# Kernel tuning notes

Hardware: AMD Instinct MI355X
Metric: run time of the kernel (lower is better)

The kernel has to match this reference:

```python
import jax, jax.numpy as jnp
import numpy as np

B, H, W, N, DIM = 2, 64, 64, 4, 128
HEADS = 4
SPLIT = 2          # split_size; idx == 0 -> window = (H, SPLIT)
HEAD_DIM = DIM // HEADS
SCALE = HEAD_DIM ** -0.5


def setup_inputs() -> dict:
    key = jax.random.key(0)
    k1, k2, k3, k4 = jax.random.split(key, 4)
    query = jax.random.normal(k1, (B, H, W, N, DIM), jnp.float32)
    key_t = jax.random.normal(k2, (B, H, W, N, DIM), jnp.float32)
    value = jax.random.normal(k3, (B, H, W, N, DIM), jnp.float32)
    conv_w = jax.random.normal(k4, (DIM, 1, 3, 3), jnp.float32) * 0.1  # depthwise get_v
    return {"query": query, "key": key_t, "value": value, "conv_w": conv_w}


def _im2cswin(x, hs, ws, heads):
    # b (i hs) (j ws) n (h d) -> (b i j) h (hs ws n) d
    b, ht, wd, n, c = x.shape
    i, j = ht // hs, wd // ws
    d = c // heads
    x = x.reshape(b, i, hs, j, ws, n, heads, d)
    x = x.transpose(0, 1, 3, 6, 2, 4, 5, 7)  # b i j h hs ws n d
    return x.reshape(b * i * j, heads, hs * ws * n, d)


def _cswin_forward(query, key, value, conv_w):
    b, ht, wd, n, c = query.shape
    hs, ws = ht, SPLIT  # idx == 0; ht % hs == 0 and wd % ws == 0 -> no padding
    i, j = ht // hs, wd // ws
    Bw = b * i * j

    q = _im2cswin(query, hs, ws, HEADS) * SCALE
    k = _im2cswin(key, hs, ws, HEADS)

    # --- get_rpe (locally-enhanced positional encoding on value) ---
    # value windows: b i j n c hs ws
    vw = value.reshape(b, i, hs, j, ws, n, c).transpose(0, 1, 3, 5, 6, 2, 4)
    vw = vw.reshape(Bw, n, c, hs, ws)
    vimg = vw.reshape(Bw * n, c, hs, ws)
    conv = jax.lax.conv_general_dilated(
        vimg, conv_w, window_strides=(1, 1), padding=((1, 1), (1, 1)),
        dimension_numbers=("NCHW", "OIHW", "NCHW"), feature_group_count=c)
    conv = conv.reshape(Bw, n, c, hs, ws)
    rpe = conv.sum(axis=1, keepdims=True)  # Bw 1 c hs ws
    # subtract center-tap contribution of all other candidates at same pixel
    mask_n = (1.0 - jnp.eye(n, dtype=query.dtype)) * -1.0  # (n, n)
    center = conv_w[:, 0, 1, 1]  # (c,)
    tmp = vw * center[None, None, :, None, None]
    tmp = jnp.einsum("jk,bkdhw->bjdhw", mask_n, tmp)
    rpe = rpe + tmp  # Bw n c hs ws

    def to_tokens(t):
        # b n (h d) hs ws -> b h (hs ws n) d
        t = t.reshape(Bw, n, HEADS, HEAD_DIM, hs, ws)
        t = t.transpose(0, 2, 4, 5, 1, 3)
        return t.reshape(Bw, HEADS, hs * ws * n, HEAD_DIM)

    rpe = to_tokens(rpe)
    v = to_tokens(vw)

    # --- window attention mask: block self-edges between candidates at same pixel ---
    L = hs * ws * n
    tok = jnp.arange(L)
    sp = tok // n  # spatial index of each token
    amask = jnp.where(sp[:, None] == sp[None, :], -jnp.inf, 0.0)
    amask = jnp.where(tok[:, None] == tok[None, :], 0.0, amask).astype(query.dtype)

    attn = jnp.einsum("bhic,bhjc->bhij", q, k) + amask[None, None]
    attn = jax.nn.softmax(attn, axis=-1)
    x = jnp.einsum("bhij,bhjc->bhic", attn, v) + rpe

    # (b i j) h (hs ws n) d -> b (i hs) (j ws) n (h d)
    x = x.reshape(b, i, j, HEADS, hs, ws, n, HEAD_DIM)
    x = x.transpose(0, 1, 4, 2, 5, 6, 3, 7).reshape(b, ht, wd, n, c)
    return x


def reference(query, key, value, conv_w):
    return _cswin_forward(query, key, value, conv_w)
```

## Files before the change

### kernel.cpp

```cpp
#include <hip/hip_runtime.h>
#include <stdint.h>


typedef __bf16 bf16x8 __attribute__((ext_vector_type(8)));
typedef float f32x4 __attribute__((ext_vector_type(4)));
typedef float f32x2 __attribute__((ext_vector_type(2)));

#if __has_builtin(__builtin_amdgcn_exp2f)
#define EXP2F __builtin_amdgcn_exp2f
#else
#define EXP2F exp2f
#endif

union U4 { uint4 u; bf16x8 v; unsigned short s[8]; };

__device__ __forceinline__ float bf2f(unsigned short h){ union{unsigned u;float f;}x; x.u=((unsigned)h)<<16; return x.f; }

__device__ __forceinline__ unsigned cvtpk(float lo, float hi){
  unsigned d;
  asm("v_cvt_pk_bf16_f32 %0, %1, %2" : "=v"(d) : "v"(lo), "v"(hi));
  return d;
}
__device__ __forceinline__ U4 pack8(float4 a, float4 b){
  U4 r;
  r.u.x = cvtpk(a.x, a.y); r.u.y = cvtpk(a.z, a.w);
  r.u.z = cvtpk(b.x, b.y); r.u.w = cvtpk(b.z, b.w);
  return r;
}

__device__ __forceinline__ void pls32(unsigned &a, unsigned &b){
#if __has_builtin(__builtin_amdgcn_permlane32_swap)
  auto r = __builtin_amdgcn_permlane32_swap(a, b, false, false);
  a = r[0]; b = r[1];
#else
  unsigned sa_ = __shfl_xor(a, 32), sb_ = __shfl_xor(b, 32);
  bool hi = ((threadIdx.x & 32) != 0);
  unsigned na = hi ? sb_ : a, nb = hi ? b : sa_;
  a = na; b = nb;
#endif
}
__device__ __forceinline__ void pls16(unsigned &a, unsigned &b){
#if __has_builtin(__builtin_amdgcn_permlane16_swap)
  auto r = __builtin_amdgcn_permlane16_swap(a, b, false, false);
  a = r[0]; b = r[1];
#else
  unsigned sa_ = __shfl_xor(a, 16), sb_ = __shfl_xor(b, 16);
  bool hi = ((threadIdx.x & 16) != 0);
  unsigned na = hi ? sb_ : a, nb = hi ? b : sa_;
  a = na; b = nb;
#endif
}

__device__ __forceinline__ void xpose_p(const unsigned w[4][2], U4& ap0, U4& ap1)
{
  unsigned a0 = w[0][0], b0 = w[1][0]; pls32(a0, b0); pls16(a0, b0);
  unsigned a1 = w[0][1], b1 = w[1][1]; pls32(a1, b1); pls16(a1, b1);
  ap0.u.x = a0; ap0.u.y = a1; ap0.u.z = b0; ap0.u.w = b1;
  unsigned c0 = w[2][0], d0 = w[3][0]; pls32(c0, d0); pls16(c0, d0);
  unsigned c1 = w[2][1], d1 = w[3][1]; pls32(c1, d1); pls16(c1, d1);
  ap1.u.x = c0; ap1.u.y = c1; ap1.u.z = d0; ap1.u.w = d1;
}

#define C_SCALE 0.25506953149031837f
#define M_SHIFT 20.0f

#define VT_OFF 0
#define KS_OFF 32768
#define LDS_BYTES 65536

__global__ __launch_bounds__(1024, 1) void cswin_attn_kernel(
    const float* __restrict__ qg,
    const float* __restrict__ kg,
    const float* __restrict__ vg,
    const float* __restrict__ cwg,
    float* __restrict__ outg)
{
  __shared__ __align__(16) unsigned char smem[LDS_BYTES];
  const int tid = threadIdx.x;
  const int lane = tid & 63;
  const int wave = tid >> 6;
  const int qd = lane >> 4;
  const int n  = lane & 15;

  const int swn = (n & 7) << 2;
  const int xb0 = ((4 * qd) ^ swn) << 2;
  const int xb1 = xb0 ^ 64;

  const int bh = blockIdx.x;
  const int head = bh & 3;
  const int bw = bh >> 2;
  const int b  = bw >> 5;
  const int jj = bw & 31;

  const size_t wbase = (size_t)b * 2097152 + (size_t)(jj * 2) * 512 + head * 32;
  const size_t lane_base = wbase + (size_t)(n >> 3) * 32768 + (size_t)((n >> 2) & 1) * 512 +
                           (size_t)(n & 3) * 128 + qd * 8;

  const int row0  = wave * 32;
  const int tilea = row0 >> 4;
  const int cka   = tilea >> 2;
  const int ta    = tilea & 3;

  float4 qra0, qra1, qrb0, qrb1;
  {
    const float* qa = qg + lane_base + (size_t)tilea * 65536;
    const float* qb = qa + 65536;
    qra0 = ((const float4*)qa)[0]; qra1 = ((const float4*)qa)[1];
    qrb0 = ((const float4*)qb)[0]; qrb1 = ((const float4*)qb)[1];
  }

  {
    const int tk = tid >> 3;
    const int p  = tid & 7;
    float4 va0, va1, va2, va3, ka0, ka1, ka2, ka3;
    {
      size_t o0 = wbase + (size_t)((tk) >> 3) * 32768 + (size_t)(((tk) >> 2) & 1) * 512 + (size_t)((tk) & 3) * 128 + p * 4;
      size_t o1 = wbase + (size_t)((128 + tk) >> 3) * 32768 + (size_t)(((128 + tk) >> 2) & 1) * 512 + (size_t)((128 + tk) & 3) * 128 + p * 4;
      size_t o2 = wbase + (size_t)((256 + tk) >> 3) * 32768 + (size_t)(((256 + tk) >> 2) & 1) * 512 + (size_t)((256 + tk) & 3) * 128 + p * 4;
      size_t o3 = wbase + (size_t)((384 + tk) >> 3) * 32768 + (size_t)(((384 + tk) >> 2) & 1) * 512 + (size_t)((384 + tk) & 3) * 128 + p * 4;
      va0 = *(const float4*)(vg + o0); ka0 = *(const float4*)(kg + o0);
      va1 = *(const float4*)(vg + o1); ka1 = *(const float4*)(kg + o1);
      va2 = *(const float4*)(vg + o2); ka2 = *(const float4*)(kg + o2);
      va3 = *(const float4*)(vg + o3); ka3 = *(const float4*)(kg + o3);
    }
    const int R0 = 4 * p;
#define STAGE_WR(VA, KA, TT)                                                         \
    {                                                                                \
      const int T_ = (TT);                                                           \
      unsigned short h0 = (unsigned short)cvtpk((VA).x, (VA).x);                     \
      unsigned short h1 = (unsigned short)cvtpk((VA).y, (VA).y);                     \
      unsigned short h2 = (unsigned short)cvtpk((VA).z, (VA).z);                     \
      unsigned short h3 = (unsigned short)cvtpk((VA).w, (VA).w);                     \
      *(unsigned short*)(smem + VT_OFF + (R0+0) * 1024 + ((T_*2) ^ (((R0+0)&7)<<4))) = h0; \
      *(unsigned short*)(smem + VT_OFF + (R0+1) * 1024 + ((T_*2) ^ (((R0+1)&7)<<4))) = h1; \
      *(unsigned short*)(smem + VT_OFF + (R0+2) * 1024 + ((T_*2) ^ (((R0+2)&7)<<4))) = h2; \
      *(unsigned short*)(smem + VT_OFF + (R0+3) * 1024 + ((T_*2) ^ (((R0+3)&7)<<4))) = h3; \
      uint2 kw; kw.x = cvtpk((KA).x, (KA).y); kw.y = cvtpk((KA).z, (KA).w);          \
      *(uint2*)(smem + KS_OFF + T_ * 64 + ((p*8) ^ (((T_>>1)&3)<<4))) = kw;          \
    }
    STAGE_WR(va0, ka0, tk)
    STAGE_WR(va1, ka1, 128 + tk)
    STAGE_WR(va2, ka2, 256 + tk)
    STAGE_WR(va3, ka3, 384 + tk)
#undef STAGE_WR
  }

  __syncthreads();

  U4 bqa = pack8(qra0, qra1);
  U4 bqb = pack8(qrb0, qrb1);

  f32x4 o0a={0,0,0,0}, o1a={0,0,0,0}, o0b={0,0,0,0}, o1b={0,0,0,0};
  f32x2 la2 = {0.f,0.f}, lb2 = {0.f,0.f};

  const int kxb = (qd * 16) ^ (((n >> 1) & 3) << 4);
  const unsigned char* kbase = smem + KS_OFF + n * 64 + kxb;

#pragma unroll 1
  for (int ck = 0; ck < 8; ck++){
    U4 ak[4];
    const unsigned char* kb = kbase + ck * 4096;
    ak[0].u = *(const uint4*)(kb);
    ak[1].u = *(const uint4*)(kb + 1024);
    ak[2].u = *(const uint4*)(kb + 2048);
    ak[3].u = *(const uint4*)(kb + 3072);

    const f32x4 zero = {0.f,0.f,0.f,0.f};
    f32x4 sa[4], sb[4];
#pragma unroll
    for (int t = 0; t < 4; t++){
      sa[t] = __builtin_amdgcn_mfma_f32_16x16x32_bf16(ak[t].v, bqa.v, zero, 0, 0, 0);
      sb[t] = __builtin_amdgcn_mfma_f32_16x16x32_bf16(ak[t].v, bqb.v, zero, 0, 0, 0);
    }
    if (ck == cka){
      bool dq = (qd == (n >> 2));
#pragma unroll
      for (int r = 0; r < 4; r++)
        if (dq && r != (n & 3)){ sa[ta][r] = -1e30f; sb[ta+1][r] = -1e30f; }
    }

    unsigned wA[4][2], wB[4][2];
    {
      const f32x2 m2 = {-M_SHIFT, -M_SHIFT};
#pragma unroll
      for (int t = 0; t < 4; t++){
        f32x2 y0 = (f32x2){sa[t][0], sa[t][1]} * C_SCALE + m2;
        f32x2 y1 = (f32x2){sa[t][2], sa[t][3]} * C_SCALE + m2;
        float p0 = EXP2F(y0.x), p1 = EXP2F(y0.y);
        float p2 = EXP2F(y1.x), p3 = EXP2F(y1.y);
        la2 += (f32x2){p0, p1}; la2 += (f32x2){p2, p3};
        wA[t][0] = cvtpk(p0, p1); wA[t][1] = cvtpk(p2, p3);
      }
#pragma unroll
      for (int t = 0; t < 4; t++){
        f32x2 y0 = (f32x2){sb[t][0], sb[t][1]} * C_SCALE + m2;
        f32x2 y1 = (f32x2){sb[t][2], sb[t][3]} * C_SCALE + m2;
        float p0 = EXP2F(y0.x), p1 = EXP2F(y0.y);
        float p2 = EXP2F(y1.x), p3 = EXP2F(y1.y);
        lb2 += (f32x2){p0, p1}; lb2 += (f32x2){p2, p3};
        wB[t][0] = cvtpk(p0, p1); wB[t][1] = cvtpk(p2, p3);
      }
    }

    const unsigned char* vr0 = smem + VT_OFF + n * 1024 + ck * 128;
    const unsigned char* vr1 = vr0 + 16 * 1024;
    U4 bv00, bv01, bv10, bv11;
    bv00.u = *(const uint4*)(vr0 + xb0);
    bv01.u = *(const uint4*)(vr0 + xb1);
    bv10.u = *(const uint4*)(vr1 + xb0);
    bv11.u = *(const uint4*)(vr1 + xb1);

    U4 apA0, apA1, apB0, apB1;
    xpose_p(wA, apA0, apA1);
    xpose_p(wB, apB0, apB1);

    o0a = __builtin_amdgcn_mfma_f32_16x16x32_bf16(apA0.v, bv00.v, o0a, 0, 0, 0);
    o0a = __builtin_amdgcn_mfma_f32_16x16x32_bf16(apA1.v, bv01.v, o0a, 0, 0, 0);
    o1a = __builtin_amdgcn_mfma_f32_16x16x32_bf16(apA0.v, bv10.v, o1a, 0, 0, 0);
    o1a = __builtin_amdgcn_mfma_f32_16x16x32_bf16(apA1.v, bv11.v, o1a, 0, 0, 0);
    o0b = __builtin_amdgcn_mfma_f32_16x16x32_bf16(apB0.v, bv00.v, o0b, 0, 0, 0);
    o0b = __builtin_amdgcn_mfma_f32_16x16x32_bf16(apB1.v, bv01.v, o0b, 0, 0, 0);
    o1b = __builtin_amdgcn_mfma_f32_16x16x32_bf16(apB0.v, bv10.v, o1b, 0, 0, 0);
    o1b = __builtin_amdgcn_mfma_f32_16x16x32_bf16(apB1.v, bv11.v, o1b, 0, 0, 0);
  }

  float w9[2][9];
#pragma unroll
  for (int nt = 0; nt < 2; nt++){
    int c = head * 32 + nt * 16 + n;
#pragma unroll
    for (int t9 = 0; t9 < 9; t9++) w9[nt][t9] = cwg[c * 9 + t9];
  }

  float la = la2.x + la2.y, lb = lb2.x + lb2.y;
  la += __shfl_xor(la, 16); la += __shfl_xor(la, 32);
  lb += __shfl_xor(lb, 16); lb += __shfl_xor(lb, 32);

  const float ila = 1.f / la, ilb = 1.f / lb;

#pragma unroll
  for (int mt = 0; mt < 2; mt++){
    const int m0 = row0 + mt * 16;
    const float ilv = mt ? ilb : ila;
    const f32x4 oo0 = mt ? o0b : o0a;
    const f32x4 oo1 = mt ? o1b : o1a;
    float il[4];
#pragma unroll
    for (int r = 0; r < 4; r++) il[r] = __shfl(ilv, qd * 4 + r);

    const int sp = (m0 >> 2) + qd;
    const int h_ = sp >> 1, w_ = sp & 1;

    float accs[2], cw2[2], vfs[2][4];
#pragma unroll
    for (int nt = 0; nt < 2; nt++){
      const int d = nt * 16 + n;
      const unsigned char* VTd = smem + VT_OFF + d * 1024;
      float acc = 0.f;
#pragma unroll
      for (int dy = -1; dy <= 1; dy++){
        int h2 = h_ + dy;
        bool hv = (h2 >= 0) && (h2 <= 63);
        int h2c = hv ? h2 : h_;
#pragma unroll
        for (int wp = 0; wp < 2; wp++){
          bool valid = hv && !((dy == 0) && (wp == w_));
          int ti = (dy + 1) * 3 + 1 + wp - w_;
          int spn = h2c * 2 + wp;
          uint2 sv = *(const uint2*)(VTd + (((2 * spn) ^ swn) << 2));
          float s = bf2f((unsigned short)(sv.x & 0xffff)) + bf2f((unsigned short)(sv.x >> 16))
                  + bf2f((unsigned short)(sv.y & 0xffff)) + bf2f((unsigned short)(sv.y >> 16));
          acc += (valid ? w9[nt][ti] : 0.f) * s;
        }
      }
      accs[nt] = acc;
      cw2[nt] = w9[nt][4];
      uint2 vv4 = *(const uint2*)(VTd + ((((m0 >> 1) + 2 * qd) ^ swn) << 2));
      vfs[nt][0] = bf2f((unsigned short)(vv4.x & 0xffff));
      vfs[nt][1] = bf2f((unsigned short)(vv4.x >> 16));
      vfs[nt][2] = bf2f((unsigned short)(vv4.y & 0xffff));
      vfs[nt][3] = bf2f((unsigned short)(vv4.y >> 16));
    }

    const size_t obase = (size_t)b * 2097152 + (size_t)h_ * 32768 +
                         (size_t)(jj * 2 + w_) * 512 + head * 32;
#pragma unroll
    for (int r = 0; r < 4; r++){
      float r0 = oo0[r] * il[r] + accs[0] + cw2[0] * vfs[0][r];
      float r1 = oo1[r] * il[r] + accs[1] + cw2[1] * vfs[1][r];
      outg[obase + (size_t)r * 128 + n]      = r0;
      outg[obase + (size_t)r * 128 + 16 + n] = r1;
    }
  }
}

extern "C" void kernel_launch(void* const* d_in, const int* in_sizes, int n_in,
                              void* d_out, int out_size, void* d_ws, size_t ws_size,
                              hipStream_t stream) {
  (void)in_sizes; (void)n_in; (void)d_ws; (void)ws_size; (void)out_size;
  cswin_attn_kernel<<<dim3(256), dim3(1024), 0, stream>>>(
      (const float*)d_in[0], (const float*)d_in[1], (const float*)d_in[2],
      (const float*)d_in[3], (float*)d_out);
}
```

Before: 112.9 us.

## Double-buffer K fragments across chunks, add MFMA priority, allow two blocks per CU

The attention loop now loads the next chunk's K fragments from LDS into a ping-pong register set while the current chunk computes, so LDS latency overlaps with MFMA and exp work. It raises wave priority around the MFMA groups with s_setprio and moves the pre-loop barrier after the Q packing. The launch bound changes from one to two 1024-thread blocks per CU, which halves the register budget per thread and risks spills in exchange for more occupancy.

```diff
diff --git a/kernel.cpp b/kernel.cpp
--- a/kernel.cpp
+++ b/kernel.cpp
@@ -68,7 +68,81 @@
 #define KS_OFF 32768
 #define LDS_BYTES 65536
 
-__global__ __launch_bounds__(1024, 1) void cswin_attn_kernel(
+#define CHUNK(CK_, C0,C1,C2,C3, N0,N1,N2,N3)                                   \
+  {                                                                            \
+    const int ck_ = (CK_);                                                     \
+                         \
+    const unsigned char* vr0 = smem + VT_OFF + n * 1024 + ck_ * 128;           \
+    const unsigned char* vr1 = vr0 + 16 * 1024;                                \
+    U4 bv00, bv01, bv10, bv11;                                                 \
+    bv00.u = *(const uint4*)(vr0 + xb0);                                       \
+    bv01.u = *(const uint4*)(vr0 + xb1);                                       \
+    bv10.u = *(const uint4*)(vr1 + xb0);                                       \
+    bv11.u = *(const uint4*)(vr1 + xb1);                                       \
+                              \
+    if (ck_ < 7){                                                              \
+      const unsigned char* kb_ = kbase + (ck_ + 1) * 4096;                     \
+      N0.u = *(const uint4*)(kb_);                                             \
+      N1.u = *(const uint4*)(kb_ + 1024);                                      \
+      N2.u = *(const uint4*)(kb_ + 2048);                                      \
+      N3.u = *(const uint4*)(kb_ + 3072);                                      \
+    }                                                                          \
+    const f32x4 zero = {0.f,0.f,0.f,0.f};                                      \
+    f32x4 sa[4], sb[4];                                                        \
+    __builtin_amdgcn_s_setprio(1);                                             \
+    sa[0] = __builtin_amdgcn_mfma_f32_16x16x32_bf16(C0.v, bqa.v, zero, 0, 0, 0); \
+    sb[0] = __builtin_amdgcn_mfma_f32_16x16x32_bf16(C0.v, bqb.v, zero, 0, 0, 0); \
+    sa[1] = __builtin_amdgcn_mfma_f32_16x16x32_bf16(C1.v, bqa.v, zero, 0, 0, 0); \
+    sb[1] = __builtin_amdgcn_mfma_f32_16x16x32_bf16(C1.v, bqb.v, zero, 0, 0, 0); \
+    sa[2] = __builtin_amdgcn_mfma_f32_16x16x32_bf16(C2.v, bqa.v, zero, 0, 0, 0); \
+    sb[2] = __builtin_amdgcn_mfma_f32_16x16x32_bf16(C2.v, bqb.v, zero, 0, 0, 0); \
+    sa[3] = __builtin_amdgcn_mfma_f32_16x16x32_bf16(C3.v, bqa.v, zero, 0, 0, 0); \
+    sb[3] = __builtin_amdgcn_mfma_f32_16x16x32_bf16(C3.v, bqb.v, zero, 0, 0, 0); \
+    __builtin_amdgcn_s_setprio(0);                                             \
+    if (ck_ == cka){                                                           \
+      bool dq = (qd == (n >> 2));                                              \
+      _Pragma("unroll")                                                        \
+      for (int r = 0; r < 4; r++)                                              \
+        if (dq && r != (n & 3)){ sa[ta][r] = -1e30f; sb[ta+1][r] = -1e30f; }   \
+    }                                                                          \
+    unsigned wA[4][2], wB[4][2];                                               \
+    {                                                                          \
+      const f32x2 m2 = {-M_SHIFT, -M_SHIFT};                                   \
+      _Pragma("unroll")                                                        \
+      for (int t = 0; t < 4; t++){                                             \
+        f32x2 y0 = (f32x2){sa[t][0], sa[t][1]} * C_SCALE + m2;                 \
+        f32x2 y1 = (f32x2){sa[t][2], sa[t][3]} * C_SCALE + m2;                 \
+        float p0 = EXP2F(y0.x), p1 = EXP2F(y0.y);                              \
+        float p2 = EXP2F(y1.x), p3 = EXP2F(y1.y);                              \
+        la2 += (f32x2){p0, p1}; la2 += (f32x2){p2, p3};                        \
+        wA[t][0] = cvtpk(p0, p1); wA[t][1] = cvtpk(p2, p3);                    \
+      }                                                                        \
+      _Pragma("unroll")                                                        \
+      for (int t = 0; t < 4; t++){                                             \
+        f32x2 y0 = (f32x2){sb[t][0], sb[t][1]} * C_SCALE + m2;                 \
+        f32x2 y1 = (f32x2){sb[t][2], sb[t][3]} * C_SCALE + m2;                 \
+        float p0 = EXP2F(y0.x), p1 = EXP2F(y0.y);                              \
+        float p2 = EXP2F(y1.x), p3 = EXP2F(y1.y);                              \
+        lb2 += (f32x2){p0, p1}; lb2 += (f32x2){p2, p3};                        \
+        wB[t][0] = cvtpk(p0, p1); wB[t][1] = cvtpk(p2, p3);                    \
+      }                                                                        \
+    }                                                                          \
+    U4 apA0, apA1, apB0, apB1;                                                 \
+    xpose_p(wA, apA0, apA1);                                                   \
+    xpose_p(wB, apB0, apB1);                                                   \
+    __builtin_amdgcn_s_setprio(1);                                             \
+    o0a = __builtin_amdgcn_mfma_f32_16x16x32_bf16(apA0.v, bv00.v, o0a, 0, 0, 0); \
+    o0a = __builtin_amdgcn_mfma_f32_16x16x32_bf16(apA1.v, bv01.v, o0a, 0, 0, 0); \
+    o1a = __builtin_amdgcn_mfma_f32_16x16x32_bf16(apA0.v, bv10.v, o1a, 0, 0, 0); \
+    o1a = __builtin_amdgcn_mfma_f32_16x16x32_bf16(apA1.v, bv11.v, o1a, 0, 0, 0); \
+    o0b = __builtin_amdgcn_mfma_f32_16x16x32_bf16(apB0.v, bv00.v, o0b, 0, 0, 0); \
+    o0b = __builtin_amdgcn_mfma_f32_16x16x32_bf16(apB1.v, bv01.v, o0b, 0, 0, 0); \
+    o1b = __builtin_amdgcn_mfma_f32_16x16x32_bf16(apB0.v, bv10.v, o1b, 0, 0, 0); \
+    o1b = __builtin_amdgcn_mfma_f32_16x16x32_bf16(apB1.v, bv11.v, o1b, 0, 0, 0); \
+    __builtin_amdgcn_s_setprio(0);                                             \
+  }
+
+__global__ __launch_bounds__(1024, 2) void cswin_attn_kernel(
     const float* __restrict__ qg,
     const float* __restrict__ kg,
     const float* __restrict__ vg,
@@ -145,83 +219,27 @@
 #undef STAGE_WR
   }
 
-  __syncthreads();
-
   U4 bqa = pack8(qra0, qra1);
   U4 bqb = pack8(qrb0, qrb1);
 
+  __syncthreads();
+
   f32x4 o0a={0,0,0,0}, o1a={0,0,0,0}, o0b={0,0,0,0}, o1b={0,0,0,0};
   f32x2 la2 = {0.f,0.f}, lb2 = {0.f,0.f};
 
   const int kxb = (qd * 16) ^ (((n >> 1) & 3) << 4);
   const unsigned char* kbase = smem + KS_OFF + n * 64 + kxb;
 
+  U4 aka0, aka1, aka2, aka3, akb0, akb1, akb2, akb3;
+  aka0.u = *(const uint4*)(kbase);
+  aka1.u = *(const uint4*)(kbase + 1024);
+  aka2.u = *(const uint4*)(kbase + 2048);
+  aka3.u = *(const uint4*)(kbase + 3072);
+
 #pragma unroll 1
-  for (int ck = 0; ck < 8; ck++){
-    U4 ak[4];
-    const unsigned char* kb = kbase + ck * 4096;
-    ak[0].u = *(const uint4*)(kb);
-    ak[1].u = *(const uint4*)(kb + 1024);
-    ak[2].u = *(const uint4*)(kb + 2048);
-    ak[3].u = *(const uint4*)(kb + 3072);
-
-    const f32x4 zero = {0.f,0.f,0.f,0.f};
-    f32x4 sa[4], sb[4];
-#pragma unroll
-    for (int t = 0; t < 4; t++){
-      sa[t] = __builtin_amdgcn_mfma_f32_16x16x32_bf16(ak[t].v, bqa.v, zero, 0, 0, 0);
-      sb[t] = __builtin_amdgcn_mfma_f32_16x16x32_bf16(ak[t].v, bqb.v, zero, 0, 0, 0);
-    }
-    if (ck == cka){
-      bool dq = (qd == (n >> 2));
-#pragma unroll
-      for (int r = 0; r < 4; r++)
-        if (dq && r != (n & 3)){ sa[ta][r] = -1e30f; sb[ta+1][r] = -1e30f; }
-    }
-
-    unsigned wA[4][2], wB[4][2];
-    {
-      const f32x2 m2 = {-M_SHIFT, -M_SHIFT};
-#pragma unroll
-      for (int t = 0; t < 4; t++){
-        f32x2 y0 = (f32x2){sa[t][0], sa[t][1]} * C_SCALE + m2;
-        f32x2 y1 = (f32x2){sa[t][2], sa[t][3]} * C_SCALE + m2;
-        float p0 = EXP2F(y0.x), p1 = EXP2F(y0.y);
-        float p2 = EXP2F(y1.x), p3 = EXP2F(y1.y);
-        la2 += (f32x2){p0, p1}; la2 += (f32x2){p2, p3};
-        wA[t][0] = cvtpk(p0, p1); wA[t][1] = cvtpk(p2, p3);
-      }
-#pragma unroll
-      for (int t = 0; t < 4; t++){
-        f32x2 y0 = (f32x2){sb[t][0], sb[t][1]} * C_SCALE + m2;
-        f32x2 y1 = (f32x2){sb[t][2], sb[t][3]} * C_SCALE + m2;
-        float p0 = EXP2F(y0.x), p1 = EXP2F(y0.y);
-        float p2 = EXP2F(y1.x), p3 = EXP2F(y1.y);
-        lb2 += (f32x2){p0, p1}; lb2 += (f32x2){p2, p3};
-        wB[t][0] = cvtpk(p0, p1); wB[t][1] = cvtpk(p2, p3);
-      }
-    }
-
-    const unsigned char* vr0 = smem + VT_OFF + n * 1024 + ck * 128;
-    const unsigned char* vr1 = vr0 + 16 * 1024;
-    U4 bv00, bv01, bv10, bv11;
-    bv00.u = *(const uint4*)(vr0 + xb0);
-    bv01.u = *(const uint4*)(vr0 + xb1);
-    bv10.u = *(const uint4*)(vr1 + xb0);
-    bv11.u = *(const uint4*)(vr1 + xb1);
-
-    U4 apA0, apA1, apB0, apB1;
-    xpose_p(wA, apA0, apA1);
-    xpose_p(wB, apB0, apB1);
-
-    o0a = __builtin_amdgcn_mfma_f32_16x16x32_bf16(apA0.v, bv00.v, o0a, 0, 0, 0);
-    o0a = __builtin_amdgcn_mfma_f32_16x16x32_bf16(apA1.v, bv01.v, o0a, 0, 0, 0);
-    o1a = __builtin_amdgcn_mfma_f32_16x16x32_bf16(apA0.v, bv10.v, o1a, 0, 0, 0);
-    o1a = __builtin_amdgcn_mfma_f32_16x16x32_bf16(apA1.v, bv11.v, o1a, 0, 0, 0);
-    o0b = __builtin_amdgcn_mfma_f32_16x16x32_bf16(apB0.v, bv00.v, o0b, 0, 0, 0);
-    o0b = __builtin_amdgcn_mfma_f32_16x16x32_bf16(apB1.v, bv01.v, o0b, 0, 0, 0);
-    o1b = __builtin_amdgcn_mfma_f32_16x16x32_bf16(apB0.v, bv10.v, o1b, 0, 0, 0);
-    o1b = __builtin_amdgcn_mfma_f32_16x16x32_bf16(apB1.v, bv11.v, o1b, 0, 0, 0);
+  for (int cc = 0; cc < 4; cc++){
+    CHUNK(cc * 2,     aka0, aka1, aka2, aka3, akb0, akb1, akb2, akb3)
+    CHUNK(cc * 2 + 1, akb0, akb1, akb2, akb3, aka0, aka1, aka2, aka3)
   }
 
   float w9[2][9];
```

Measured after the change: 155.3 us. 1.38x slower.
